# Kernel optimization log

Hardware: AMD Instinct MI355X
Metric: run time of the kernel (lower is better)

Reference implementation:

```python
import jax, jax.numpy as jnp
import numpy as np

# Differentiable logic gates on {0,1}-valued floats (standard soft-gate forms
# used by QuantizedSAE's XOR/AND/OR modules):
#   XOR(a,b) = a + b - 2ab,  AND(a,b) = ab,  OR(a,b) = a + b - ab

def _xor(a, b):
    return a + b - 2.0 * a * b

def _and(a, b):
    return a * b

def _or(a, b):
    return a + b - a * b

def _full_adder(a, b, c_in):
    s1 = _xor(a, b)
    c1 = _and(a, b)
    s = _xor(s1, c_in)
    c2 = _and(s1, c_in)
    return s, _or(c1, c2)

def _ripple_carry_adder(x, y):
    # x, y: (batch, n_bits). Bit-serial scan LSB->MSB with carry dependency.
    # Note: full adder with c_in=0 reduces exactly to the half adder used at i=0.
    def step(c, ab):
        a, b = ab
        s, c_out = _full_adder(a, b, c)
        return c_out, (s, c_out)
    c0 = jnp.zeros(x.shape[0], x.dtype)
    _, (s, c) = jax.lax.scan(step, c0, (x.T, y.T))  # scan over n_bits
    return s.T, c.T  # each (batch, n_bits)

def _csa_forward(x, mask):
    # x: (batch, len_x, n_bits); mask: (len_x,) int. len_x >= 3 path.
    B = x.shape[0]
    in0 = x[:, 0]       # (batch, n_bits)
    t_carry = x[:, 1]   # (batch, n_bits)
    carry = jnp.zeros(B, x.dtype)

    def step(state, inp):
        in0, t_carry, carry = state
        xi, m = inp                     # xi: (batch, n_bits), m: scalar int
        keep = m > 0
        s, c = _full_adder(in0, xi, t_carry)
        overflow = jax.lax.stop_gradient(c[:, -1])  # detached MSB carry
        carry = carry + jnp.where(keep, overflow, jnp.zeros_like(overflow))
        rolled = jnp.roll(c, 1, axis=-1).at[:, 0].set(0.0)  # shift carries up one bit
        in0 = jnp.where(keep, s, in0)
        t_carry = jnp.where(keep, rolled, t_carry)
        return (in0, t_carry, carry), None

    xs = (jnp.swapaxes(x[:, 2:], 0, 1), mask[2:])  # scan over the len_x-2 summands
    (in0, t_carry, carry), _ = jax.lax.scan(step, (in0, t_carry, carry), xs)

    output, rc = _ripple_carry_adder(in0, t_carry)
    carry = carry + jax.lax.stop_gradient(rc[:, -1])
    return output, carry

def setup_inputs() -> dict:
    key = jax.random.key(0)
    B, L, NBITS = 32768, 64, 16
    u = jax.random.uniform(key, (B, L, NBITS), dtype=jnp.float32)
    x = (u < 0.5).astype(jnp.float32)  # random bits in {0,1}
    mask = jnp.ones((L,), dtype=jnp.int32)
    return {"x": x, "mask": mask}

def reference(x, mask):
    return _csa_forward(x, mask)
```

## Files before the change

### kernel.cpp

```cpp
#include <hip/hip_runtime.h>


__device__ __forceinline__ unsigned pack16(const float4* __restrict__ p) {
    float4 f0 = p[0], f1 = p[1], f2 = p[2], f3 = p[3];
    float acc = f0.x;
    acc = fmaf(f0.y,     2.f, acc);
    acc = fmaf(f0.z,     4.f, acc);
    acc = fmaf(f0.w,     8.f, acc);
    acc = fmaf(f1.x,    16.f, acc);
    acc = fmaf(f1.y,    32.f, acc);
    acc = fmaf(f1.z,    64.f, acc);
    acc = fmaf(f1.w,   128.f, acc);
    acc = fmaf(f2.x,   256.f, acc);
    acc = fmaf(f2.y,   512.f, acc);
    acc = fmaf(f2.z,  1024.f, acc);
    acc = fmaf(f2.w,  2048.f, acc);
    acc = fmaf(f3.x,  4096.f, acc);
    acc = fmaf(f3.y,  8192.f, acc);
    acc = fmaf(f3.z, 16384.f, acc);
    acc = fmaf(f3.w, 32768.f, acc);
    return (unsigned)acc;
}

__global__ __launch_bounds__(256) void csa_pack(const float* __restrict__ x,
                                                unsigned short* __restrict__ packed,
                                                int n_slices) {
    int t = blockIdx.x * 256 + threadIdx.x;
    if (t >= n_slices) return;
    const float4* p = reinterpret_cast<const float4*>(x) + (size_t)t * 4;
    packed[t] = (unsigned short)pack16(p);
}

__global__ __launch_bounds__(256) void csa_scan64(const unsigned short* __restrict__ packed,
                                                  const int* __restrict__ mask,
                                                  float* __restrict__ out,
                                                  float* __restrict__ carry_out,
                                                  int B) {
    int r = blockIdx.x * 256 + threadIdx.x;

    unsigned long long keepmask = __ballot(mask[threadIdx.x & 63] > 0);

    if (r >= B) return;

    const uint4* p = reinterpret_cast<const uint4*>(packed + (size_t)r * 64);
    unsigned w[32];
#pragma unroll
    for (int k = 0; k < 8; ++k) {
        uint4 v = p[k];
        w[4 * k + 0] = v.x; w[4 * k + 1] = v.y;
        w[4 * k + 2] = v.z; w[4 * k + 3] = v.w;
    }

    unsigned in0 = w[0] & 0xFFFFu;
    unsigned tc  = (w[0] >> 16) & 0xFFFFu;
    unsigned cnt = 0;

#pragma unroll
    for (int i = 2; i < 64; ++i) {
        unsigned xi = (w[i >> 1] >> ((i & 1) * 16)) & 0xFFFFu;
        unsigned s  = in0 ^ xi ^ tc;
        unsigned c  = (in0 & xi) | (tc & (in0 | xi));
        if ((keepmask >> i) & 1ull) {
            cnt += (c >> 15) & 1u;
            in0 = s;
            tc  = (c << 1) & 0xFFFFu;
        }
    }

    unsigned sum = in0 + tc;
    cnt += (sum >> 16) & 1u;

    float4* orow = reinterpret_cast<float4*>(out + (size_t)r * 16);
#pragma unroll
    for (int q = 0; q < 4; ++q) {
        float4 o;
        o.x = (float)((sum >> (q * 4 + 0)) & 1u);
        o.y = (float)((sum >> (q * 4 + 1)) & 1u);
        o.z = (float)((sum >> (q * 4 + 2)) & 1u);
        o.w = (float)((sum >> (q * 4 + 3)) & 1u);
        orow[q] = o;
    }
    carry_out[r] = (float)cnt;
}

__global__ __launch_bounds__(256) void csa_fused(const float* __restrict__ x,
                                                 const int* __restrict__ mask,
                                                 float* __restrict__ out,
                                                 float* __restrict__ carry_out,
                                                 int B, int L) {
    int r = blockIdx.x * 256 + threadIdx.x;
    if (r >= B) return;
    const float4* row = reinterpret_cast<const float4*>(x) + (size_t)r * L * 4;

    unsigned in0 = pack16(row);
    unsigned tc  = pack16(row + 4);
    unsigned cnt = 0;
    for (int i = 2; i < L; ++i) {
        unsigned xi = pack16(row + (size_t)i * 4);
        unsigned s  = in0 ^ xi ^ tc;
        unsigned c  = (in0 & xi) | (tc & (in0 | xi));
        if (mask[i] > 0) {
            cnt += (c >> 15) & 1u;
            in0 = s;
            tc  = (c << 1) & 0xFFFFu;
        }
    }
    unsigned sum = in0 + tc;
    cnt += (sum >> 16) & 1u;

    float4* orow = reinterpret_cast<float4*>(out + (size_t)r * 16);
#pragma unroll
    for (int q = 0; q < 4; ++q) {
        float4 o;
        o.x = (float)((sum >> (q * 4 + 0)) & 1u);
        o.y = (float)((sum >> (q * 4 + 1)) & 1u);
        o.z = (float)((sum >> (q * 4 + 2)) & 1u);
        o.w = (float)((sum >> (q * 4 + 3)) & 1u);
        orow[q] = o;
    }
    carry_out[r] = (float)cnt;
}

extern "C" void kernel_launch(void* const* d_in, const int* in_sizes, int n_in,
                              void* d_out, int out_size, void* d_ws, size_t ws_size,
                              hipStream_t stream) {
    const float* x    = (const float*)d_in[0];
    const int*   mask = (const int*)d_in[1];
    float*       out  = (float*)d_out;

    const int L = in_sizes[1];
    const int B = in_sizes[0] / (L * 16);
    float* carry_out = out + (size_t)B * 16;

    const size_t n_slices = (size_t)B * L;
    const size_t need     = n_slices * sizeof(unsigned short);

    if (L == 64 && (B % 256) == 0 && ws_size >= need) {
        unsigned short* packed = (unsigned short*)d_ws;
        csa_pack<<<dim3((unsigned)((n_slices + 255) / 256)), dim3(256), 0, stream>>>(
            x, packed, (int)n_slices);
        csa_scan64<<<dim3((unsigned)((B + 255) / 256)), dim3(256), 0, stream>>>(
            packed, mask, out, carry_out, B);
    } else {
        csa_fused<<<dim3((unsigned)((B + 255) / 256)), dim3(256), 0, stream>>>(
            x, mask, out, carry_out, B, L);
    }
}
```

Measured before the change: 190.0 us.

## Fuse bit-packing and carry-save scan into one block kernel via shared memory

Replaces the two-kernel pipeline (pack floats to 16-bit words in a global workspace, then scan) with one kernel. Each block of 256 threads loads 32 rows with coalesced float4 reads, builds nibbles with wave shuffles, and stores the packed words in padded shared memory. The first 32 threads then run the 64-step carry-save scan. This removes the workspace write and read-back and one kernel launch. In exchange only 32 of 256 threads do the scan phase, so the serial scan may limit overlap with loads.

```diff
diff --git a/kernel.cpp b/kernel.cpp
--- a/kernel.cpp
+++ b/kernel.cpp
@@ -1,5 +1,82 @@
 #include <hip/hip_runtime.h>
 
+
+#define RPB 32
+#define LSTRIDE 68
+
+__global__ __launch_bounds__(256) void csa_fused_block(const float* __restrict__ x,
+                                                       const int* __restrict__ mask,
+                                                       float* __restrict__ out,
+                                                       float* __restrict__ carry_out,
+                                                       int B) {
+    unsigned long long keepmask = __ballot(mask[threadIdx.x & 63] > 0);
+
+    __shared__ unsigned short sl[RPB * LSTRIDE];
+
+    const int r0 = blockIdx.x * RPB;
+    const float4* base = reinterpret_cast<const float4*>(x) + (size_t)r0 * 256;
+
+#pragma unroll 4
+    for (int it = 0; it < (RPB * 256) / 256; ++it) {
+        int idx = it * 256 + (int)threadIdx.x;
+        float4 f = base[idx];
+        unsigned nib = (f.x != 0.f ? 1u : 0u) | (f.y != 0.f ? 2u : 0u)
+                     | (f.z != 0.f ? 4u : 0u) | (f.w != 0.f ? 8u : 0u);
+        int q = idx & 3;
+        unsigned v = nib << (q * 4);
+        v |= __shfl_xor(v, 1);
+        v |= __shfl_xor(v, 2);
+        if (q == 0) {
+            int s  = idx >> 2;
+            int rr = s >> 6, si = s & 63;
+            sl[rr * LSTRIDE + si] = (unsigned short)v;
+        }
+    }
+    __syncthreads();
+
+    int tid = threadIdx.x;
+    if (tid < RPB) {
+        const uint2* rp = reinterpret_cast<const uint2*>(&sl[tid * LSTRIDE]);
+        unsigned w[32];
+#pragma unroll
+        for (int k = 0; k < 16; ++k) {
+            uint2 v = rp[k];
+            w[2 * k] = v.x; w[2 * k + 1] = v.y;
+        }
+
+        unsigned in0 = w[0] & 0xFFFFu;
+        unsigned tc  = (w[0] >> 16) & 0xFFFFu;
+        unsigned cnt = 0;
+
+#pragma unroll
+        for (int i = 2; i < 64; ++i) {
+            unsigned xi = (w[i >> 1] >> ((i & 1) * 16)) & 0xFFFFu;
+            unsigned s  = in0 ^ xi ^ tc;
+            unsigned c  = (in0 & xi) | (tc & (in0 | xi));
+            if ((keepmask >> i) & 1ull) {
+                cnt += (c >> 15) & 1u;
+                in0 = s;
+                tc  = (c << 1) & 0xFFFFu;
+            }
+        }
+
+        unsigned sum = in0 + tc;
+        cnt += (sum >> 16) & 1u;
+
+        int r = r0 + tid;
+        float4* orow = reinterpret_cast<float4*>(out + (size_t)r * 16);
+#pragma unroll
+        for (int q = 0; q < 4; ++q) {
+            float4 o;
+            o.x = (float)((sum >> (q * 4 + 0)) & 1u);
+            o.y = (float)((sum >> (q * 4 + 1)) & 1u);
+            o.z = (float)((sum >> (q * 4 + 2)) & 1u);
+            o.w = (float)((sum >> (q * 4 + 3)) & 1u);
+            orow[q] = o;
+        }
+        carry_out[r] = (float)cnt;
+    }
+}
 
 __device__ __forceinline__ unsigned pack16(const float4* __restrict__ p) {
     float4 f0 = p[0], f1 = p[1], f2 = p[2], f3 = p[3];
@@ -20,67 +97,6 @@
     acc = fmaf(f3.z, 16384.f, acc);
     acc = fmaf(f3.w, 32768.f, acc);
     return (unsigned)acc;
-}
-
-__global__ __launch_bounds__(256) void csa_pack(const float* __restrict__ x,
-                                                unsigned short* __restrict__ packed,
-                                                int n_slices) {
-    int t = blockIdx.x * 256 + threadIdx.x;
-    if (t >= n_slices) return;
-    const float4* p = reinterpret_cast<const float4*>(x) + (size_t)t * 4;
-    packed[t] = (unsigned short)pack16(p);
-}
-
-__global__ __launch_bounds__(256) void csa_scan64(const unsigned short* __restrict__ packed,
-                                                  const int* __restrict__ mask,
-                                                  float* __restrict__ out,
-                                                  float* __restrict__ carry_out,
-                                                  int B) {
-    int r = blockIdx.x * 256 + threadIdx.x;
-
-    unsigned long long keepmask = __ballot(mask[threadIdx.x & 63] > 0);
-
-    if (r >= B) return;
-
-    const uint4* p = reinterpret_cast<const uint4*>(packed + (size_t)r * 64);
-    unsigned w[32];
-#pragma unroll
-    for (int k = 0; k < 8; ++k) {
-        uint4 v = p[k];
-        w[4 * k + 0] = v.x; w[4 * k + 1] = v.y;
-        w[4 * k + 2] = v.z; w[4 * k + 3] = v.w;
-    }
-
-    unsigned in0 = w[0] & 0xFFFFu;
-    unsigned tc  = (w[0] >> 16) & 0xFFFFu;
-    unsigned cnt = 0;
-
-#pragma unroll
-    for (int i = 2; i < 64; ++i) {
-        unsigned xi = (w[i >> 1] >> ((i & 1) * 16)) & 0xFFFFu;
-        unsigned s  = in0 ^ xi ^ tc;
-        unsigned c  = (in0 & xi) | (tc & (in0 | xi));
-        if ((keepmask >> i) & 1ull) {
-            cnt += (c >> 15) & 1u;
-            in0 = s;
-            tc  = (c << 1) & 0xFFFFu;
-        }
-    }
-
-    unsigned sum = in0 + tc;
-    cnt += (sum >> 16) & 1u;
-
-    float4* orow = reinterpret_cast<float4*>(out + (size_t)r * 16);
-#pragma unroll
-    for (int q = 0; q < 4; ++q) {
-        float4 o;
-        o.x = (float)((sum >> (q * 4 + 0)) & 1u);
-        o.y = (float)((sum >> (q * 4 + 1)) & 1u);
-        o.z = (float)((sum >> (q * 4 + 2)) & 1u);
-        o.w = (float)((sum >> (q * 4 + 3)) & 1u);
-        orow[q] = o;
-    }
-    carry_out[r] = (float)cnt;
 }
 
 __global__ __launch_bounds__(256) void csa_fused(const float* __restrict__ x,
@@ -132,15 +148,9 @@
     const int B = in_sizes[0] / (L * 16);
     float* carry_out = out + (size_t)B * 16;
 
-    const size_t n_slices = (size_t)B * L;
-    const size_t need     = n_slices * sizeof(unsigned short);
-
-    if (L == 64 && (B % 256) == 0 && ws_size >= need) {
-        unsigned short* packed = (unsigned short*)d_ws;
-        csa_pack<<<dim3((unsigned)((n_slices + 255) / 256)), dim3(256), 0, stream>>>(
-            x, packed, (int)n_slices);
-        csa_scan64<<<dim3((unsigned)((B + 255) / 256)), dim3(256), 0, stream>>>(
-            packed, mask, out, carry_out, B);
+    if (L == 64 && (B % RPB) == 0) {
+        csa_fused_block<<<dim3(B / RPB), dim3(256), 0, stream>>>(
+            x, mask, out, carry_out, B);
     } else {
         csa_fused<<<dim3((unsigned)((B + 255) / 256)), dim3(256), 0, stream>>>(
             x, mask, out, carry_out, B, L);
```

New measurement: 190.9 us. Within noise of the previous version (+0.5%).
